# Optimization experiments

Measured on AMD Instinct MI355X. Metric: run time of the kernel, lower is better.

Reference implementation:

```python
import jax, jax.numpy as jnp
import numpy as np

E, F, NF = 16, 128, 64          # elevators, per-elevator feature size, num_floors
PRE, CI, CH, OUT = 64, 64, 32, 128
R, DROPOFF = 3, 0.333


def _cell(x, h, c, Wih, Whh, bih, bhh, alpha=1.0):
    # torch LSTM cell; alpha scales the candidate-state update (alpha-LSTM).
    g = x @ Wih.T + bih + h @ Whh.T + bhh
    i, f, gg, o = jnp.split(g, 4, axis=-1)
    c2 = jax.nn.sigmoid(f) * c + alpha * jax.nn.sigmoid(i) * jnp.tanh(gg)
    h2 = jax.nn.sigmoid(o) * jnp.tanh(c2)
    return h2, c2


def _forward(features, pre_h, pre_c, out_h, out_c,
             pre_Wih0, pre_Whh0, pre_bih0, pre_bhh0,
             pre_Wih1, pre_Whh1, pre_bih1, pre_bhh1,
             fc_W, fc_b,
             comm_Wih0, comm_Whh0, comm_bih0, comm_bhh0,
             comm_Wih1, comm_Whh1, comm_bih1, comm_bhh1,
             out_Wih, out_Whh, out_bih, out_bhh,
             tar_W, tar_b, dir_W, dir_b):
    # alpha schedule: round r uses dropoff**r, same alpha for all E elevators in a round
    alphas = jnp.repeat(jnp.float32(DROPOFF) ** jnp.arange(R, dtype=jnp.float32), E)

    def step(carry, feat_t):
        ph, pc, oh, oc = carry                       # [E,2,PRE] x2, [E,OUT] x2
        feat = feat_t.reshape(E, F)
        # 2-layer preprocess LSTM, seq len 1, vectorized over elevators
        h0, c0 = _cell(feat, ph[:, 0], pc[:, 0], pre_Wih0, pre_Whh0, pre_bih0, pre_bhh0)
        h1, c1 = _cell(h0,   ph[:, 1], pc[:, 1], pre_Wih1, pre_Whh1, pre_bih1, pre_bhh1)
        x = jax.nn.leaky_relu(h1 @ fc_W.T + fc_b, 0.05)   # [E, CI]
        # sequential communication: rounds x elevators through shared alpha-LSTM state
        xs = jnp.tile(x, (R, 1))                          # [R*E, CI]
        z = jnp.zeros((CH,), feat.dtype)

        def comm_step(cst, xi_a):
            ch0, cc0, ch1, cc1 = cst
            xi, a = xi_a
            nh0, nc0 = _cell(xi, ch0, cc0, comm_Wih0, comm_Whh0, comm_bih0, comm_bhh0, a)
            nh1, nc1 = _cell(nh0, ch1, cc1, comm_Wih1, comm_Whh1, comm_bih1, comm_bhh1, a)
            return (nh0, nc0, nh1, nc1), None

        (ch0, cc0, ch1, cc1), _ = jax.lax.scan(comm_step, (z, z, z, z), (xs, alphas))
        group = jnp.concatenate([cc0, cc1])               # comm cell state flattened [2*CH]
        # postprocessing LSTM (1 layer) + heads, per elevator
        out_in = jnp.concatenate([jnp.broadcast_to(group, (E, 2 * CH)), feat], axis=1)
        noh, noc = _cell(out_in, oh, oc, out_Wih, out_Whh, out_bih, out_bhh)
        tar = jax.nn.softmax(noh @ tar_W.T + tar_b, axis=-1)
        dire = jax.nn.softmax(noh @ dir_W.T + dir_b, axis=-1)
        out = jnp.concatenate([tar, dire], axis=1)        # [E, NF+3]
        new_carry = (jnp.stack([h0, h1], 1), jnp.stack([c0, c1], 1), noh, noc)
        return new_carry, out

    _, outs = jax.lax.scan(step, (pre_h, pre_c, out_h, out_c), features)
    return outs  # [B, E, NF+3]


def setup_inputs() -> dict:
    key = jax.random.key(0)
    ks = iter(jax.random.split(key, 40))

    def p(shape, fan):
        return jax.random.uniform(next(ks), shape, jnp.float32, -1.0, 1.0) / np.sqrt(fan)

    B = 2048
    return {
        "features": jax.random.normal(next(ks), (B, E * F), jnp.float32),
        "pre_h": jnp.zeros((E, 2, PRE), jnp.float32),
        "pre_c": jnp.zeros((E, 2, PRE), jnp.float32),
        "out_h": jnp.zeros((E, OUT), jnp.float32),
        "out_c": jnp.zeros((E, OUT), jnp.float32),
        "pre_Wih0": p((4 * PRE, F), PRE), "pre_Whh0": p((4 * PRE, PRE), PRE),
        "pre_bih0": p((4 * PRE,), PRE), "pre_bhh0": p((4 * PRE,), PRE),
        "pre_Wih1": p((4 * PRE, PRE), PRE), "pre_Whh1": p((4 * PRE, PRE), PRE),
        "pre_bih1": p((4 * PRE,), PRE), "pre_bhh1": p((4 * PRE,), PRE),
        "fc_W": p((CI, PRE), PRE), "fc_b": p((CI,), PRE),
        "comm_Wih0": p((4 * CH, CI), CH), "comm_Whh0": p((4 * CH, CH), CH),
        "comm_bih0": p((4 * CH,), CH), "comm_bhh0": p((4 * CH,), CH),
        "comm_Wih1": p((4 * CH, CH), CH), "comm_Whh1": p((4 * CH, CH), CH),
        "comm_bih1": p((4 * CH,), CH), "comm_bhh1": p((4 * CH,), CH),
        "out_Wih": p((4 * OUT, F + 2 * CH), OUT), "out_Whh": p((4 * OUT, OUT), OUT),
        "out_bih": p((4 * OUT,), OUT), "out_bhh": p((4 * OUT,), OUT),
        "tar_W": p((NF, OUT), OUT), "tar_b": p((NF,), OUT),
        "dir_W": p((3, OUT), OUT), "dir_b": p((3,), OUT),
    }


def reference(features, pre_h, pre_c, out_h, out_c,
              pre_Wih0, pre_Whh0, pre_bih0, pre_bhh0,
              pre_Wih1, pre_Whh1, pre_bih1, pre_bhh1,
              fc_W, fc_b,
              comm_Wih0, comm_Whh0, comm_bih0, comm_bhh0,
              comm_Wih1, comm_Whh1, comm_bih1, comm_bhh1,
              out_Wih, out_Whh, out_bih, out_bhh,
              tar_W, tar_b, dir_W, dir_b):
    return _forward(features, pre_h, pre_c, out_h, out_c,
                    pre_Wih0, pre_Whh0, pre_bih0, pre_bhh0,
                    pre_Wih1, pre_Whh1, pre_bih1, pre_bhh1,
                    fc_W, fc_b,
                    comm_Wih0, comm_Whh0, comm_bih0, comm_bhh0,
                    comm_Wih1, comm_Whh1, comm_bih1, comm_bhh1,
                    out_Wih, out_Whh, out_bih, out_bhh,
                    tar_W, tar_b, dir_W, dir_b)
```

## Files before the change

kernel.cpp:

```cpp
#include <hip/hip_runtime.h>
#include <hip/hip_bf16.h>


#define E_ 16
#define F_ 128

typedef int i4 __attribute__((ext_vector_type(4)));
typedef _Float16 hf;
typedef hf hf2 __attribute__((ext_vector_type(2)));

__device__ __forceinline__ float sigf(float x) { return 1.0f / (1.0f + __expf(-x)); }
__device__ __forceinline__ float tanhf_(float x) {
  float e = __expf(2.0f * x);
  return 1.0f - 2.0f / (e + 1.0f);
}
__device__ __forceinline__ float lane_bcast(float v, int k) {
  return __int_as_float(__builtin_amdgcn_readlane(__float_as_int(v), k));
}
__device__ __forceinline__ float fdot2(int a, int b, float c) {
#if __has_builtin(__builtin_amdgcn_fdot2)
  return __builtin_amdgcn_fdot2(__builtin_bit_cast(hf2, a),
                                __builtin_bit_cast(hf2, b), c, false);
#else
  float d;
  asm("v_dot2_f32_f16 %0, %1, %2, %3" : "=v"(d) : "v"(a), "v"(b), "v"(c));
  return d;
#endif
}

#define LDS_BARRIER()                                        \
  do {                                                       \
    asm volatile("s_waitcnt lgkmcnt(0)" ::: "memory");       \
    __builtin_amdgcn_s_barrier();                            \
    __builtin_amdgcn_sched_barrier(0);                       \
  } while (0)

__global__ void f2h_kernel(const float* __restrict__ src, hf* __restrict__ dst, int n) {
  int i = blockIdx.x * 256 + threadIdx.x;
  if (i < n) dst[i] = (hf)src[i];
}

__global__ __launch_bounds__(256) void gemm_k(
    const float* __restrict__ A, int lda,
    const float* __restrict__ W, int ldw, int co,
    const float* __restrict__ b1, const float* __restrict__ b2,
    float* __restrict__ C, int N, int K) {
  __shared__ float As[64 * 65];
  __shared__ float Ws[128 * 65];
  const int tid = threadIdx.x;
  const int m0 = blockIdx.x * 64;
  const int n0 = blockIdx.y * 128;
  const int rr = tid >> 4;
  const int c4 = (tid & 15) << 2;
  const int tm = tid >> 4;
  const int tn = tid & 15;

  float acc[4][8];
#pragma unroll
  for (int i = 0; i < 4; ++i)
#pragma unroll
    for (int j = 0; j < 8; ++j) acc[i][j] = 0.0f;

  for (int kk = 0; kk < K; kk += 64) {
#pragma unroll
    for (int p = 0; p < 4; ++p) {
      const int r = rr + p * 16;
      const float4 v = *(const float4*)(A + (size_t)(m0 + r) * lda + kk + c4);
      float* dst = &As[r * 65 + c4];
      dst[0] = v.x; dst[1] = v.y; dst[2] = v.z; dst[3] = v.w;
    }
#pragma unroll
    for (int p = 0; p < 8; ++p) {
      const int n = rr + p * 16;
      const float4 v = *(const float4*)(W + (size_t)(n0 + n) * ldw + co + kk + c4);
      float* dst = &Ws[n * 65 + c4];
      dst[0] = v.x; dst[1] = v.y; dst[2] = v.z; dst[3] = v.w;
    }
    __syncthreads();
#pragma unroll 4
    for (int k = 0; k < 64; ++k) {
      float a[4], wv[8];
#pragma unroll
      for (int i = 0; i < 4; ++i) a[i] = As[(tm * 4 + i) * 65 + k];
#pragma unroll
      for (int j = 0; j < 8; ++j) wv[j] = Ws[(tn * 8 + j) * 65 + k];
#pragma unroll
      for (int i = 0; i < 4; ++i)
#pragma unroll
        for (int j = 0; j < 8; ++j) acc[i][j] += a[i] * wv[j];
    }
    __syncthreads();
  }
#pragma unroll
  for (int i = 0; i < 4; ++i) {
    const int m = m0 + tm * 4 + i;
#pragma unroll
    for (int j = 0; j < 8; ++j) {
      const int n = n0 + tn * 8 + j;
      float v = acc[i][j];
      if (b1) v += b1[n];
      if (b2) v += b2[n];
      C[(size_t)m * N + n] = v;
    }
  }
}

__global__ __launch_bounds__(576) void k2_pre(
    const float* __restrict__ pg0, const float* __restrict__ preh,
    const float* __restrict__ prec,
    const hf* __restrict__ hWhh0, const hf* __restrict__ hWih1,
    const hf* __restrict__ hWhh1, const hf* __restrict__ hfcW,
    const float* __restrict__ bih1, const float* __restrict__ bhh1,
    const float* __restrict__ fcb, float* __restrict__ xout, int B) {
  const int e = blockIdx.x, tid = threadIdx.x;
  const int wv = tid >> 6, l = tid & 63, cls = l >> 4, sub = l & 15;
  __shared__ __align__(16) hf h0s[2][64];
  __shared__ __align__(16) hf h1s[2][64];

  int wa[32], wb[32];
  float bias = 0.f, c = 0.f;
  const float* pgp = nullptr;
  int j = 0;

  if (wv < 4) {
    j = wv * 16 + sub;
    const int r = cls * 64 + j;
    const i4* p0 = (const i4*)(hWhh0 + r * 64);
#pragma unroll
    for (int i = 0; i < 8; ++i) {
      i4 a = p0[i]; wa[4*i]=a.x; wa[4*i+1]=a.y; wa[4*i+2]=a.z; wa[4*i+3]=a.w;
    }
    pgp = pg0 + (size_t)e * 256 + r;
    if (cls == 1) { c = prec[e * 128 + j]; h0s[1][j] = (hf)preh[e * 128 + j]; }
  } else if (wv < 8) {
    j = (wv - 4) * 16 + sub;
    const int r = cls * 64 + j;
    const i4* p1 = (const i4*)(hWih1 + r * 64);
    const i4* p2 = (const i4*)(hWhh1 + r * 64);
#pragma unroll
    for (int i = 0; i < 8; ++i) {
      i4 a = p1[i]; wa[4*i]=a.x; wa[4*i+1]=a.y; wa[4*i+2]=a.z; wa[4*i+3]=a.w;
      i4 b = p2[i]; wb[4*i]=b.x; wb[4*i+1]=b.y; wb[4*i+2]=b.z; wb[4*i+3]=b.w;
    }
    bias = bih1[r] + bhh1[r];
    if (cls == 1) { c = prec[e * 128 + 64 + j]; h1s[1][j] = (hf)preh[e * 128 + 64 + j]; }
  } else {
    j = l;
    const i4* pf = (const i4*)(hfcW + l * 64);
#pragma unroll
    for (int i = 0; i < 8; ++i) {
      i4 a = pf[i]; wa[4*i]=a.x; wa[4*i+1]=a.y; wa[4*i+2]=a.z; wa[4*i+3]=a.w;
    }
    bias = fcb[l];
  }
  __syncthreads();

  auto doL0 = [&](int nn, float pgv) {
    const i4* hp = (const i4*)h0s[(nn + 1) & 1];
    float a0 = 0.f, a1 = 0.f, a2 = 0.f, a3 = 0.f;
#pragma unroll
    for (int i = 0; i < 8; ++i) {
      i4 h = hp[i];
      a0 = fdot2(wa[4*i],   h.x, a0); a1 = fdot2(wa[4*i+1], h.y, a1);
      a2 = fdot2(wa[4*i+2], h.z, a2); a3 = fdot2(wa[4*i+3], h.w, a3);
    }
    const float pre = (a0 + a1) + (a2 + a3) + pgv;
    const float act = (cls == 2) ? tanhf_(pre) : sigf(pre);
    const float p32 = __shfl_xor(act, 32);
    const float ig = act * p32;
    const float p16 = __shfl_xor(ig, 16);
    if (cls == 1) {
      c = act * c + p16;
      h0s[nn & 1][j] = (hf)(p32 * tanhf_(c));
    }
  };
  auto doL1 = [&](int nn) {
    const i4* hp0 = (const i4*)h0s[(nn + 1) & 1];
    const i4* hp1 = (const i4*)h1s[nn & 1];
    float a0 = 0.f, a1 = 0.f, a2 = 0.f, a3 = 0.f;
#pragma unroll
    for (int i = 0; i < 8; ++i) {
      i4 h = hp0[i];
      a0 = fdot2(wa[4*i],   h.x, a0); a1 = fdot2(wa[4*i+1], h.y, a1);
      a2 = fdot2(wa[4*i+2], h.z, a2); a3 = fdot2(wa[4*i+3], h.w, a3);
    }
#pragma unroll
    for (int i = 0; i < 8; ++i) {
      i4 h = hp1[i];
      a0 = fdot2(wb[4*i],   h.x, a0); a1 = fdot2(wb[4*i+1], h.y, a1);
      a2 = fdot2(wb[4*i+2], h.z, a2); a3 = fdot2(wb[4*i+3], h.w, a3);
    }
    const float pre = (a0 + a1) + (a2 + a3) + bias;
    const float act = (cls == 2) ? tanhf_(pre) : sigf(pre);
    const float p32 = __shfl_xor(act, 32);
    const float ig = act * p32;
    const float p16 = __shfl_xor(ig, 16);
    if (cls == 1) {
      c = act * c + p16;
      h1s[(nn + 1) & 1][j] = (hf)(p32 * tanhf_(c));
    }
  };
  auto doFC = [&](int nn) {
    const i4* hp1 = (const i4*)h1s[nn & 1];
    float a0 = 0.f, a1 = 0.f, a2 = 0.f, a3 = 0.f;
#pragma unroll
    for (int i = 0; i < 8; ++i) {
      i4 h = hp1[i];
      a0 = fdot2(wa[4*i],   h.x, a0); a1 = fdot2(wa[4*i+1], h.y, a1);
      a2 = fdot2(wa[4*i+2], h.z, a2); a3 = fdot2(wa[4*i+3], h.w, a3);
    }
    const float xv = (a0 + a1) + (a2 + a3) + bias;
    xout[((size_t)(nn - 2) * E_ + e) * 64 + l] = (xv > 0.f) ? xv : 0.05f * xv;
  };

  float pr0 = 0.f, pr1 = 0.f, pr2 = 0.f, pr3 = 0.f;
  if (wv < 4) {
    pr0 = (0 < B) ? pgp[0] : 0.f;
    pr1 = (1 < B) ? pgp[(size_t)4096] : 0.f;
    pr2 = (2 < B) ? pgp[(size_t)2 * 4096] : 0.f;
    pr3 = (3 < B) ? pgp[(size_t)3 * 4096] : 0.f;
  }
  const int NT = (B + 2 + 3) & ~3;

#define K2SUB(KK, PR)                                                \
  {                                                                  \
    const int nn = n + KK;                                           \
    if (wv < 4) {                                                    \
      if (nn < B) doL0(nn, PR);                                      \
      PR = (nn + 4 < B) ? pgp[(size_t)(nn + 4) * 4096] : 0.f;        \
    } else if (wv < 8) {                                             \
      if (nn >= 1 && nn <= B) doL1(nn);                              \
    } else {                                                         \
      if (nn >= 2 && nn < B + 2) doFC(nn);                           \
    }                                                                \
    LDS_BARRIER();                                                   \
  }

  for (int n = 0; n < NT; n += 4) {
    K2SUB(0, pr0)
    K2SUB(1, pr1)
    K2SUB(2, pr2)
    K2SUB(3, pr3)
  }
#undef K2SUB
}

__global__ __launch_bounds__(256) void k3_comm(
    const float* __restrict__ gih0, const float* __restrict__ Whh0,
    const float* __restrict__ Wih1, const float* __restrict__ Whh1,
    const float* __restrict__ bih1, const float* __restrict__ bhh1,
    float* __restrict__ grp, int B) {
  const int w = threadIdx.x >> 6;
  const int l = threadIdx.x & 63;
  const int t = blockIdx.x * 4 + w;

  float wh0a[32], wh0b[32], wi1a[32], wi1b[32], wh1a[32], wh1b[32];
#pragma unroll
  for (int i = 0; i < 32; ++i) {
    wh0a[i] = Whh0[l * 32 + i];         wh0b[i] = Whh0[(l + 64) * 32 + i];
    wi1a[i] = Wih1[l * 32 + i];         wi1b[i] = Wih1[(l + 64) * 32 + i];
    wh1a[i] = Whh1[l * 32 + i];         wh1b[i] = Whh1[(l + 64) * 32 + i];
  }
  const float cb1a = bih1[l] + bhh1[l];
  const float cb1b = bih1[l + 64] + bhh1[l + 64];

  float h0 = 0.0f, c0 = 0.0f, h1 = 0.0f, c1 = 0.0f;
  float al = 1.0f;
  const float* gbase = gih0 + (size_t)t * (E_ * 128);
  for (int r = 0; r < 3; ++r) {
    for (int e = 0; e < E_; ++e) {
      float ga = gbase[e * 128 + l];
      float gb = gbase[e * 128 + l + 64];
#pragma unroll
      for (int k = 0; k < 32; ++k) {
        const float hv = lane_bcast(h0, k);
        ga += wh0a[k] * hv;
        gb += wh0b[k] * hv;
      }
      {
        const float fa = __shfl_xor(ga, 32);
        const float ob = __shfl_xor(gb, 32);
        c0 = sigf(fa) * c0 + al * sigf(ga) * tanhf_(gb);
        h0 = sigf(ob) * tanhf_(c0);
      }
      float ga1 = cb1a, gb1 = cb1b;
#pragma unroll
      for (int k = 0; k < 32; ++k) {
        const float hv = lane_bcast(h0, k);
        ga1 += wi1a[k] * hv;
        gb1 += wi1b[k] * hv;
      }
#pragma unroll
      for (int k = 0; k < 32; ++k) {
        const float hv = lane_bcast(h1, k);
        ga1 += wh1a[k] * hv;
        gb1 += wh1b[k] * hv;
      }
      {
        const float fa = __shfl_xor(ga1, 32);
        const float ob = __shfl_xor(gb1, 32);
        c1 = sigf(fa) * c1 + al * sigf(ga1) * tanhf_(gb1);
        h1 = sigf(ob) * tanhf_(c1);
      }
    }
    al *= 0.333f;
  }
  if (l < 32) {
    grp[(size_t)t * 64 + l] = c0;
    grp[(size_t)t * 64 + 32 + l] = c1;
  }
}

__global__ __launch_bounds__(512) void k4_out(
    const float* __restrict__ pgo, const float* __restrict__ gg,
    const float* __restrict__ outh, const float* __restrict__ outc,
    const hf* __restrict__ hWo, float* __restrict__ noh, int B) {
  const int e = blockIdx.x, tid = threadIdx.x;
  const int wv = tid >> 6, l = tid & 63, cls = l >> 4, sub = l & 15;
  const int j = wv * 16 + sub;
  const int r = cls * 128 + j;
  __shared__ __align__(16) hf hs[2][128];

  int w[64];
  {
    const i4* pw = (const i4*)(hWo + (size_t)r * 128);
#pragma unroll
    for (int i = 0; i < 16; ++i) {
      i4 a = pw[i]; w[4*i]=a.x; w[4*i+1]=a.y; w[4*i+2]=a.z; w[4*i+3]=a.w;
    }
  }
  float c = 0.f;
  if (cls == 1) { c = outc[e * 128 + j]; hs[1][j] = (hf)outh[e * 128 + j]; }
  __syncthreads();

  const float* pgoP = pgo + (size_t)e * 512 + r;
  const float* ggP  = gg + r;

  auto doStep = [&](int nn, float po, float gv) {
    const i4* hp = (const i4*)hs[(nn + 1) & 1];
    float a0 = 0.f, a1 = 0.f, a2 = 0.f, a3 = 0.f;
#pragma unroll
    for (int i = 0; i < 16; ++i) {
      i4 h = hp[i];
      a0 = fdot2(w[4*i],   h.x, a0); a1 = fdot2(w[4*i+1], h.y, a1);
      a2 = fdot2(w[4*i+2], h.z, a2); a3 = fdot2(w[4*i+3], h.w, a3);
    }
    const float pre = (a0 + a1) + (a2 + a3) + po + gv;
    const float act = (cls == 2) ? tanhf_(pre) : sigf(pre);
    const float p32 = __shfl_xor(act, 32);
    const float ig = act * p32;
    const float p16 = __shfl_xor(ig, 16);
    if (cls == 1) {
      c = act * c + p16;
      const float h = p32 * tanhf_(c);
      hs[nn & 1][j] = (hf)h;
      noh[((size_t)nn * E_ + e) * 128 + j] = h;
    }
  };

  float po0 = (0 < B) ? pgoP[0] : 0.f;
  float po1 = (1 < B) ? pgoP[(size_t)8192] : 0.f;
  float po2 = (2 < B) ? pgoP[(size_t)2 * 8192] : 0.f;
  float po3 = (3 < B) ? pgoP[(size_t)3 * 8192] : 0.f;
  float g0 = (0 < B) ? ggP[0] : 0.f;
  float g1 = (1 < B) ? ggP[(size_t)512] : 0.f;
  float g2 = (2 < B) ? ggP[(size_t)2 * 512] : 0.f;
  float g3 = (3 < B) ? ggP[(size_t)3 * 512] : 0.f;
  const int NT = (B + 3) & ~3;

#define K4SUB(KK, PO, GV)                                            \
  {                                                                  \
    const int nn = n + KK;                                           \
    if (nn < B) doStep(nn, PO, GV);                                  \
    PO = (nn + 4 < B) ? pgoP[(size_t)(nn + 4) * 8192] : 0.f;         \
    GV = (nn + 4 < B) ? ggP[(size_t)(nn + 4) * 512] : 0.f;           \
    LDS_BARRIER();                                                   \
  }

  for (int n = 0; n < NT; n += 4) {
    K4SUB(0, po0, g0)
    K4SUB(1, po1, g1)
    K4SUB(2, po2, g2)
    K4SUB(3, po3, g3)
  }
#undef K4SUB
}

__global__ __launch_bounds__(256) void k5_heads(
    const float* __restrict__ noh, const float* __restrict__ tarW,
    const float* __restrict__ tarb, const float* __restrict__ dirW,
    const float* __restrict__ dirb, float* __restrict__ out) {
  __shared__ float tw[128 * 64];
  __shared__ float tb[64];
  const int tid = threadIdx.x;
  for (int idx = tid; idx < 8192; idx += 256) {
    const int j = idx >> 7, k = idx & 127;
    tw[k * 64 + j] = tarW[idx];
  }
  if (tid < 64) tb[tid] = tarb[tid];
  __syncthreads();
  const int w = tid >> 6, l = tid & 63;
  const float db0 = dirb[0], db1 = dirb[1], db2 = dirb[2];

  for (int p = 0; p < 16; ++p) {
    const int row = blockIdx.x * 64 + p * 4 + w;
    const float na = noh[(size_t)row * 128 + l];
    const float nb = noh[(size_t)row * 128 + 64 + l];
    float acc = tb[l];
#pragma unroll
    for (int k = 0; k < 64; ++k) acc += tw[k * 64 + l] * lane_bcast(na, k);
#pragma unroll
    for (int k = 0; k < 64; ++k) acc += tw[(64 + k) * 64 + l] * lane_bcast(nb, k);
    float m = acc;
#pragma unroll
    for (int s = 32; s; s >>= 1) m = fmaxf(m, __shfl_xor(m, s));
    const float ex = __expf(acc - m);
    float sm = ex;
#pragma unroll
    for (int s = 32; s; s >>= 1) sm += __shfl_xor(sm, s);
    out[(size_t)row * 67 + l] = ex / sm;
    float d0 = dirW[l] * na + dirW[64 + l] * nb;
    float d1 = dirW[128 + l] * na + dirW[192 + l] * nb;
    float d2 = dirW[256 + l] * na + dirW[320 + l] * nb;
#pragma unroll
    for (int s = 32; s; s >>= 1) {
      d0 += __shfl_xor(d0, s);
      d1 += __shfl_xor(d1, s);
      d2 += __shfl_xor(d2, s);
    }
    d0 += db0; d1 += db1; d2 += db2;
    const float dm = fmaxf(d0, fmaxf(d1, d2));
    const float e0 = __expf(d0 - dm), e1 = __expf(d1 - dm), e2 = __expf(d2 - dm);
    const float ds = e0 + e1 + e2;
    if (l < 3) out[(size_t)row * 67 + 64 + l] = (l == 0 ? e0 : (l == 1 ? e1 : e2)) / ds;
  }
}

extern "C" void kernel_launch(void* const* d_in, const int* in_sizes, int n_in,
                              void* d_out, int out_size, void* d_ws, size_t ws_size,
                              hipStream_t stream) {
  const float* features = (const float*)d_in[0];
  const float* pre_h    = (const float*)d_in[1];
  const float* pre_c    = (const float*)d_in[2];
  const float* out_h    = (const float*)d_in[3];
  const float* out_c    = (const float*)d_in[4];
  const float* pre_Wih0 = (const float*)d_in[5];
  const float* pre_Whh0 = (const float*)d_in[6];
  const float* pre_bih0 = (const float*)d_in[7];
  const float* pre_bhh0 = (const float*)d_in[8];
  const float* pre_Wih1 = (const float*)d_in[9];
  const float* pre_Whh1 = (const float*)d_in[10];
  const float* pre_bih1 = (const float*)d_in[11];
  const float* pre_bhh1 = (const float*)d_in[12];
  const float* fc_W     = (const float*)d_in[13];
  const float* fc_b     = (const float*)d_in[14];
  const float* comm_Wih0 = (const float*)d_in[15];
  const float* comm_Whh0 = (const float*)d_in[16];
  const float* comm_bih0 = (const float*)d_in[17];
  const float* comm_bhh0 = (const float*)d_in[18];
  const float* comm_Wih1 = (const float*)d_in[19];
  const float* comm_Whh1 = (const float*)d_in[20];
  const float* comm_bih1 = (const float*)d_in[21];
  const float* comm_bhh1 = (const float*)d_in[22];
  const float* out_Wih  = (const float*)d_in[23];
  const float* out_Whh  = (const float*)d_in[24];
  const float* out_bih  = (const float*)d_in[25];
  const float* out_bhh  = (const float*)d_in[26];
  const float* tar_W    = (const float*)d_in[27];
  const float* tar_b    = (const float*)d_in[28];
  const float* dir_W    = (const float*)d_in[29];
  const float* dir_b    = (const float*)d_in[30];

  const int B = in_sizes[0] / (E_ * F_);
  float* ws = (float*)d_ws;
  float* pg0 = ws;
  float* pgo = pg0 + (size_t)B * E_ * 256;
  float* xbf = pgo + (size_t)B * E_ * 512;
  float* gih = xbf + (size_t)B * E_ * 64;
  float* grp = gih + (size_t)B * E_ * 128;
  float* gg  = grp + (size_t)B * 64;
  float* noh = gg + (size_t)B * 512;
  hf* hWhh0 = (hf*)(noh + (size_t)B * E_ * 128);
  hf* hWih1 = hWhh0 + 256 * 64;
  hf* hWhh1 = hWih1 + 256 * 64;
  hf* hfcW  = hWhh1 + 256 * 64;
  hf* hWo   = hfcW + 64 * 64;
  (void)ws_size; (void)n_in; (void)out_size;

  f2h_kernel<<<(256 * 64 + 255) / 256, 256, 0, stream>>>(pre_Whh0, hWhh0, 256 * 64);
  f2h_kernel<<<(256 * 64 + 255) / 256, 256, 0, stream>>>(pre_Wih1, hWih1, 256 * 64);
  f2h_kernel<<<(256 * 64 + 255) / 256, 256, 0, stream>>>(pre_Whh1, hWhh1, 256 * 64);
  f2h_kernel<<<(64 * 64 + 255) / 256, 256, 0, stream>>>(fc_W, hfcW, 64 * 64);
  f2h_kernel<<<(512 * 128 + 255) / 256, 256, 0, stream>>>(out_Whh, hWo, 512 * 128);

  const int MB = B * E_ / 64;

  gemm_k<<<dim3(MB, 2), 256, 0, stream>>>(features, 128, pre_Wih0, 128, 0,
                                          pre_bih0, pre_bhh0, pg0, 256, 128);
  gemm_k<<<dim3(MB, 4), 256, 0, stream>>>(features, 128, out_Wih, 192, 64,
                                          out_bih, out_bhh, pgo, 512, 128);
  k2_pre<<<E_, 576, 0, stream>>>(pg0, pre_h, pre_c, hWhh0, hWih1, hWhh1, hfcW,
                                 pre_bih1, pre_bhh1, fc_b, xbf, B);
  gemm_k<<<dim3(MB, 1), 256, 0, stream>>>(xbf, 64, comm_Wih0, 64, 0,
                                          comm_bih0, comm_bhh0, gih, 128, 64);
  k3_comm<<<B / 4, 256, 0, stream>>>(gih, comm_Whh0, comm_Wih1, comm_Whh1,
                                     comm_bih1, comm_bhh1, grp, B);
  gemm_k<<<dim3(B / 64, 4), 256, 0, stream>>>(grp, 64, out_Wih, 192, 0,
                                              nullptr, nullptr, gg, 512, 64);
  k4_out<<<E_, 512, 0, stream>>>(pgo, gg, out_h, out_c, hWo, noh, B);
  k5_heads<<<B * E_ / 64, 256, 0, stream>>>(noh, tar_W, tar_b, dir_W, dir_b,
                                            (float*)d_out);
}
```

Measured before the change: 3.574 ms.

## Broadcast hidden state via readlane, fold FC into layer-0 waves, branchless gate activation

The recurrent kernels now have each lane load one packed half2 of the hidden state from LDS and broadcast it with readlane as a scalar operand to the dot products, replacing per-lane vector LDS reads. The FC head is merged into the layer-0 waves, so the preprocess kernel drops from 9 to 8 waves. Gate activations use a single branchless exp-based formula for both sigmoid and tanh. Launch bounds gain occupancy hints, and the barrier drops its scheduling fence. The aim is lower LDS traffic and shorter serial step latency, at the cost of many scalar readlanes per step and extra FC work on the layer-0 waves.

```diff
diff --git a/kernel.cpp b/kernel.cpp
--- a/kernel.cpp
+++ b/kernel.cpp
@@ -28,11 +28,18 @@
 #endif
 }
 
-#define LDS_BARRIER()                                        \
-  do {                                                       \
-    asm volatile("s_waitcnt lgkmcnt(0)" ::: "memory");       \
-    __builtin_amdgcn_s_barrier();                            \
-    __builtin_amdgcn_sched_barrier(0);                       \
+__device__ __forceinline__ float gate_act(float pre, int cls) {
+  const float bb = (cls == 2) ? 2.0f : -1.0f;
+  const float aa = (cls == 2) ? -2.0f : 1.0f;
+  const float dd = (cls == 2) ? 1.0f : 0.0f;
+  return dd + aa / (1.0f + __expf(bb * pre));
+}
+
+#define LDS_BARRIER()                                      \
+  do {                                                     \
+    asm volatile("s_waitcnt lgkmcnt(0)" ::: "memory");     \
+    __builtin_amdgcn_s_barrier();                          \
+    asm volatile("" ::: "memory");                         \
   } while (0)
 
 __global__ void f2h_kernel(const float* __restrict__ src, hf* __restrict__ dst, int n) {
@@ -105,7 +112,7 @@
   }
 }
 
-__global__ __launch_bounds__(576) void k2_pre(
+__global__ __launch_bounds__(512, 2) void k2_pre(
     const float* __restrict__ pg0, const float* __restrict__ preh,
     const float* __restrict__ prec,
     const hf* __restrict__ hWhh0, const hf* __restrict__ hWih1,
@@ -114,27 +121,29 @@
     const float* __restrict__ fcb, float* __restrict__ xout, int B) {
   const int e = blockIdx.x, tid = threadIdx.x;
   const int wv = tid >> 6, l = tid & 63, cls = l >> 4, sub = l & 15;
-  __shared__ __align__(16) hf h0s[2][64];
-  __shared__ __align__(16) hf h1s[2][64];
+  const bool isA = (wv < 4);
+  const int wg = isA ? wv : (wv - 4);
+  const int j = wg * 16 + sub;
+  const int r = cls * 64 + j;
+  __shared__ __align__(8) hf h0s[2][64];
+  __shared__ __align__(8) hf h1s[2][64];
 
   int wa[32], wb[32];
-  float bias = 0.f, c = 0.f;
+  float bias = 0.f, fbias = 0.f, c = 0.f;
   const float* pgp = nullptr;
-  int j = 0;
-
-  if (wv < 4) {
-    j = wv * 16 + sub;
-    const int r = cls * 64 + j;
+
+  if (isA) {
     const i4* p0 = (const i4*)(hWhh0 + r * 64);
+    const i4* pf = (const i4*)(hfcW + j * 64);
 #pragma unroll
     for (int i = 0; i < 8; ++i) {
       i4 a = p0[i]; wa[4*i]=a.x; wa[4*i+1]=a.y; wa[4*i+2]=a.z; wa[4*i+3]=a.w;
-    }
+      i4 b = pf[i]; wb[4*i]=b.x; wb[4*i+1]=b.y; wb[4*i+2]=b.z; wb[4*i+3]=b.w;
+    }
+    fbias = fcb[j];
     pgp = pg0 + (size_t)e * 256 + r;
     if (cls == 1) { c = prec[e * 128 + j]; h0s[1][j] = (hf)preh[e * 128 + j]; }
-  } else if (wv < 8) {
-    j = (wv - 4) * 16 + sub;
-    const int r = cls * 64 + j;
+  } else {
     const i4* p1 = (const i4*)(hWih1 + r * 64);
     const i4* p2 = (const i4*)(hWhh1 + r * 64);
 #pragma unroll
@@ -144,28 +153,23 @@
     }
     bias = bih1[r] + bhh1[r];
     if (cls == 1) { c = prec[e * 128 + 64 + j]; h1s[1][j] = (hf)preh[e * 128 + 64 + j]; }
-  } else {
-    j = l;
-    const i4* pf = (const i4*)(hfcW + l * 64);
-#pragma unroll
-    for (int i = 0; i < 8; ++i) {
-      i4 a = pf[i]; wa[4*i]=a.x; wa[4*i+1]=a.y; wa[4*i+2]=a.z; wa[4*i+3]=a.w;
-    }
-    bias = fcb[l];
   }
   __syncthreads();
 
   auto doL0 = [&](int nn, float pgv) {
-    const i4* hp = (const i4*)h0s[(nn + 1) & 1];
+    const int vh0 = ((const int*)h0s[(nn + 1) & 1])[l & 31];
     float a0 = 0.f, a1 = 0.f, a2 = 0.f, a3 = 0.f;
 #pragma unroll
-    for (int i = 0; i < 8; ++i) {
-      i4 h = hp[i];
-      a0 = fdot2(wa[4*i],   h.x, a0); a1 = fdot2(wa[4*i+1], h.y, a1);
-      a2 = fdot2(wa[4*i+2], h.z, a2); a3 = fdot2(wa[4*i+3], h.w, a3);
+    for (int k = 0; k < 32; k += 4) {
+      const int s0 = __builtin_amdgcn_readlane(vh0, k);
+      const int s1 = __builtin_amdgcn_readlane(vh0, k + 1);
+      const int s2 = __builtin_amdgcn_readlane(vh0, k + 2);
+      const int s3 = __builtin_amdgcn_readlane(vh0, k + 3);
+      a0 = fdot2(wa[k], s0, a0);     a1 = fdot2(wa[k + 1], s1, a1);
+      a2 = fdot2(wa[k + 2], s2, a2); a3 = fdot2(wa[k + 3], s3, a3);
     }
     const float pre = (a0 + a1) + (a2 + a3) + pgv;
-    const float act = (cls == 2) ? tanhf_(pre) : sigf(pre);
+    const float act = gate_act(pre, cls);
     const float p32 = __shfl_xor(act, 32);
     const float ig = act * p32;
     const float p16 = __shfl_xor(ig, 16);
@@ -174,24 +178,46 @@
       h0s[nn & 1][j] = (hf)(p32 * tanhf_(c));
     }
   };
+  auto doFC = [&](int nn) {
+    const int vh1 = ((const int*)h1s[nn & 1])[l & 31];
+    float a0 = 0.f, a1 = 0.f, a2 = 0.f, a3 = 0.f;
+#pragma unroll
+    for (int k = 0; k < 32; k += 4) {
+      const int s0 = __builtin_amdgcn_readlane(vh1, k);
+      const int s1 = __builtin_amdgcn_readlane(vh1, k + 1);
+      const int s2 = __builtin_amdgcn_readlane(vh1, k + 2);
+      const int s3 = __builtin_amdgcn_readlane(vh1, k + 3);
+      a0 = fdot2(wb[k], s0, a0);     a1 = fdot2(wb[k + 1], s1, a1);
+      a2 = fdot2(wb[k + 2], s2, a2); a3 = fdot2(wb[k + 3], s3, a3);
+    }
+    const float xv = (a0 + a1) + (a2 + a3) + fbias;
+    if (cls == 0)
+      xout[((size_t)(nn - 2) * E_ + e) * 64 + j] = (xv > 0.f) ? xv : 0.05f * xv;
+  };
   auto doL1 = [&](int nn) {
-    const i4* hp0 = (const i4*)h0s[(nn + 1) & 1];
-    const i4* hp1 = (const i4*)h1s[nn & 1];
+    const int vh0 = ((const int*)h0s[(nn + 1) & 1])[l & 31];
+    const int vh1 = ((const int*)h1s[nn & 1])[l & 31];
     float a0 = 0.f, a1 = 0.f, a2 = 0.f, a3 = 0.f;
 #pragma unroll
-    for (int i = 0; i < 8; ++i) {
-      i4 h = hp0[i];
-      a0 = fdot2(wa[4*i],   h.x, a0); a1 = fdot2(wa[4*i+1], h.y, a1);
-      a2 = fdot2(wa[4*i+2], h.z, a2); a3 = fdot2(wa[4*i+3], h.w, a3);
-    }
-#pragma unroll
-    for (int i = 0; i < 8; ++i) {
-      i4 h = hp1[i];
-      a0 = fdot2(wb[4*i],   h.x, a0); a1 = fdot2(wb[4*i+1], h.y, a1);
-      a2 = fdot2(wb[4*i+2], h.z, a2); a3 = fdot2(wb[4*i+3], h.w, a3);
+    for (int k = 0; k < 32; k += 4) {
+      const int s0 = __builtin_amdgcn_readlane(vh0, k);
+      const int s1 = __builtin_amdgcn_readlane(vh0, k + 1);
+      const int s2 = __builtin_amdgcn_readlane(vh0, k + 2);
+      const int s3 = __builtin_amdgcn_readlane(vh0, k + 3);
+      a0 = fdot2(wa[k], s0, a0);     a1 = fdot2(wa[k + 1], s1, a1);
+      a2 = fdot2(wa[k + 2], s2, a2); a3 = fdot2(wa[k + 3], s3, a3);
+    }
+#pragma unroll
+    for (int k = 0; k < 32; k += 4) {
+      const int s0 = __builtin_amdgcn_readlane(vh1, k);
+      const int s1 = __builtin_amdgcn_readlane(vh1, k + 1);
+      const int s2 = __builtin_amdgcn_readlane(vh1, k + 2);
+      const int s3 = __builtin_amdgcn_readlane(vh1, k + 3);
+      a0 = fdot2(wb[k], s0, a0);     a1 = fdot2(wb[k + 1], s1, a1);
+      a2 = fdot2(wb[k + 2], s2, a2); a3 = fdot2(wb[k + 3], s3, a3);
     }
     const float pre = (a0 + a1) + (a2 + a3) + bias;
-    const float act = (cls == 2) ? tanhf_(pre) : sigf(pre);
+    const float act = gate_act(pre, cls);
     const float p32 = __shfl_xor(act, 32);
     const float ig = act * p32;
     const float p16 = __shfl_xor(ig, 16);
@@ -200,21 +226,9 @@
       h1s[(nn + 1) & 1][j] = (hf)(p32 * tanhf_(c));
     }
   };
-  auto doFC = [&](int nn) {
-    const i4* hp1 = (const i4*)h1s[nn & 1];
-    float a0 = 0.f, a1 = 0.f, a2 = 0.f, a3 = 0.f;
-#pragma unroll
-    for (int i = 0; i < 8; ++i) {
-      i4 h = hp1[i];
-      a0 = fdot2(wa[4*i],   h.x, a0); a1 = fdot2(wa[4*i+1], h.y, a1);
-      a2 = fdot2(wa[4*i+2], h.z, a2); a3 = fdot2(wa[4*i+3], h.w, a3);
-    }
-    const float xv = (a0 + a1) + (a2 + a3) + bias;
-    xout[((size_t)(nn - 2) * E_ + e) * 64 + l] = (xv > 0.f) ? xv : 0.05f * xv;
-  };
 
   float pr0 = 0.f, pr1 = 0.f, pr2 = 0.f, pr3 = 0.f;
-  if (wv < 4) {
+  if (isA) {
     pr0 = (0 < B) ? pgp[0] : 0.f;
     pr1 = (1 < B) ? pgp[(size_t)4096] : 0.f;
     pr2 = (2 < B) ? pgp[(size_t)2 * 4096] : 0.f;
@@ -225,13 +239,12 @@
 #define K2SUB(KK, PR)                                                \
   {                                                                  \
     const int nn = n + KK;                                           \
-    if (wv < 4) {                                                    \
+    if (isA) {                                                       \
       if (nn < B) doL0(nn, PR);                                      \
       PR = (nn + 4 < B) ? pgp[(size_t)(nn + 4) * 4096] : 0.f;        \
-    } else if (wv < 8) {                                             \
+      if (nn >= 2 && nn < B + 2) doFC(nn);                           \
+    } else {                                                         \
       if (nn >= 1 && nn <= B) doL1(nn);                              \
-    } else {                                                         \
-      if (nn >= 2 && nn < B + 2) doFC(nn);                           \
     }                                                                \
     LDS_BARRIER();                                                   \
   }
@@ -245,7 +258,7 @@
 #undef K2SUB
 }
 
-__global__ __launch_bounds__(256) void k3_comm(
+__global__ __launch_bounds__(256, 1) void k3_comm(
     const float* __restrict__ gih0, const float* __restrict__ Whh0,
     const float* __restrict__ Wih1, const float* __restrict__ Whh1,
     const float* __restrict__ bih1, const float* __restrict__ bhh1,
@@ -311,7 +324,7 @@
   }
 }
 
-__global__ __launch_bounds__(512) void k4_out(
+__global__ __launch_bounds__(512, 2) void k4_out(
     const float* __restrict__ pgo, const float* __restrict__ gg,
     const float* __restrict__ outh, const float* __restrict__ outc,
     const hf* __restrict__ hWo, float* __restrict__ noh, int B) {
@@ -319,7 +332,7 @@
   const int wv = tid >> 6, l = tid & 63, cls = l >> 4, sub = l & 15;
   const int j = wv * 16 + sub;
   const int r = cls * 128 + j;
-  __shared__ __align__(16) hf hs[2][128];
+  __shared__ __align__(8) hf hs[2][128];
 
   int w[64];
   {
@@ -337,16 +350,19 @@
   const float* ggP  = gg + r;
 
   auto doStep = [&](int nn, float po, float gv) {
-    const i4* hp = (const i4*)hs[(nn + 1) & 1];
+    const int vh = ((const int*)hs[(nn + 1) & 1])[l];
     float a0 = 0.f, a1 = 0.f, a2 = 0.f, a3 = 0.f;
 #pragma unroll
-    for (int i = 0; i < 16; ++i) {
-      i4 h = hp[i];
-      a0 = fdot2(w[4*i],   h.x, a0); a1 = fdot2(w[4*i+1], h.y, a1);
-      a2 = fdot2(w[4*i+2], h.z, a2); a3 = fdot2(w[4*i+3], h.w, a3);
+    for (int k = 0; k < 64; k += 4) {
+      const int s0 = __builtin_amdgcn_readlane(vh, k);
+      const int s1 = __builtin_amdgcn_readlane(vh, k + 1);
+      const int s2 = __builtin_amdgcn_readlane(vh, k + 2);
+      const int s3 = __builtin_amdgcn_readlane(vh, k + 3);
+      a0 = fdot2(w[k], s0, a0);     a1 = fdot2(w[k + 1], s1, a1);
+      a2 = fdot2(w[k + 2], s2, a2); a3 = fdot2(w[k + 3], s3, a3);
     }
     const float pre = (a0 + a1) + (a2 + a3) + po + gv;
-    const float act = (cls == 2) ? tanhf_(pre) : sigf(pre);
+    const float act = gate_act(pre, cls);
     const float p32 = __shfl_xor(act, 32);
     const float ig = act * p32;
     const float p16 = __shfl_xor(ig, 16);
@@ -499,7 +515,7 @@
                                           pre_bih0, pre_bhh0, pg0, 256, 128);
   gemm_k<<<dim3(MB, 4), 256, 0, stream>>>(features, 128, out_Wih, 192, 64,
                                           out_bih, out_bhh, pgo, 512, 128);
-  k2_pre<<<E_, 576, 0, stream>>>(pg0, pre_h, pre_c, hWhh0, hWih1, hWhh1, hfcW,
+  k2_pre<<<E_, 512, 0, stream>>>(pg0, pre_h, pre_c, hWhh0, hWih1, hWhh1, hfcW,
                                  pre_bih1, pre_bhh1, fc_b, xbf, B);
   gemm_k<<<dim3(MB, 1), 256, 0, stream>>>(xbf, 64, comm_Wih0, 64, 0,
                                           comm_bih0, comm_bhh0, gih, 128, 64);
```

Result: slower. 4.017 ms (+12.4%).
